# Optimization experiments

Hardware: AMD Instinct MI355X
Metric: run time of the kernel (lower is better)

## Reference

```python
import jax, jax.numpy as jnp
import numpy as np

B, S, DIM, H = 4, 2048, 1024, 16
HD = DIM // H
SCALE = HD ** -0.5


def setup_inputs() -> dict:
    key = jax.random.key(0)
    ks = jax.random.split(key, 7)
    init = 0.02
    return {
        "query": jax.random.normal(ks[0], (B, S, DIM), dtype=jnp.float32),
        "key": jax.random.normal(ks[1], (B, S, DIM), dtype=jnp.float32),
        "value": jax.random.normal(ks[2], (B, S, DIM), dtype=jnp.float32),
        "attn_mask": jnp.tril(jnp.ones((S, S), dtype=bool)),
        "Wq": jax.random.normal(ks[3], (DIM, DIM), dtype=jnp.float32) * init,
        "Wk": jax.random.normal(ks[4], (DIM, DIM), dtype=jnp.float32) * init,
        "Wv": jax.random.normal(ks[5], (DIM, DIM), dtype=jnp.float32) * init,
        "Wo": jax.random.normal(ks[6], (DIM, DIM), dtype=jnp.float32) * init,
    }


def _heads(x):
    # [B,S,DIM] -> [B,H,S,HD]
    b, s, _ = x.shape
    return x.reshape(b, s, H, HD).transpose(0, 2, 1, 3)


def reference(query, key, value, attn_mask, Wq, Wk, Wv, Wo):
    # nn.Linear: x @ W.T (weights here stored as [out,in])
    q = _heads(query @ Wq.T)
    k = _heads(key @ Wk.T)
    v = _heads(value @ Wv.T)
    logits = jnp.einsum("bhqd,bhkd->bhqk", q, k) * SCALE
    mask = attn_mask[None, None, :, :]  # broadcast to [B,H,S,S]
    masked = jnp.where(mask, logits, -1e9)
    weights = jax.nn.softmax(masked, axis=-1)
    weights = weights * mask.astype(weights.dtype)
    denom = jnp.maximum(weights.sum(axis=-1, keepdims=True), 1e-9)
    weights = weights / denom
    out = jnp.einsum("bhqk,bhkd->bhqd", weights, v)
    out = out.transpose(0, 2, 1, 3).reshape(query.shape[0], query.shape[1], -1)
    return out @ Wo.T
```

## Files before the change

kernel.cpp:

```cpp
#include <hip/hip_runtime.h>
#include <hip/hip_bf16.h>
#include <cstdio>

typedef __attribute__((ext_vector_type(8))) short bf16x8;
typedef __attribute__((ext_vector_type(4))) float f32x4;
typedef unsigned short u16;
typedef unsigned int u32;

__device__ inline u16 f2bf(float f) {
    union { float f; u32 u; } x; x.f = f;
    u32 u = x.u;
    u32 r = (u + 0x7fffu + ((u >> 16) & 1u)) >> 16;
    return (u16)r;
}

__device__ inline float exp2_fast(float x) {
    float r;
    asm("v_exp_f32 %0, %1" : "=v"(r) : "v"(x));
    return r;
}

__global__ __launch_bounds__(256) void convf2b(const float* __restrict__ s,
                                               u16* __restrict__ d, int n4) {
    int i = blockIdx.x * 256 + threadIdx.x;
    if (i >= n4) return;
    float4 v = reinterpret_cast<const float4*>(s)[i];
    ushort4 o;
    o.x = f2bf(v.x); o.y = f2bf(v.y); o.z = f2bf(v.z); o.w = f2bf(v.w);
    reinterpret_cast<ushort4*>(d)[i] = o;
}

template <int MODE>
__global__ __launch_bounds__(256) void gemm_bt(const u16* __restrict__ A,
                                               const u16* __restrict__ Bw,
                                               void* __restrict__ Cout, float scale) {
    __shared__ u16 As[128 * 64];
    __shared__ u16 Bs[128 * 64];
    const int tid = threadIdx.x;
    const int lane = tid & 63;
    const int w = tid >> 6;
    const int wr = w >> 1, wc = w & 1;
    const int gm = blockIdx.y * 128;
    const int gn = blockIdx.x * 128;

    f32x4 acc[4][4];
#pragma unroll
    for (int m = 0; m < 4; ++m)
#pragma unroll
        for (int n = 0; n < 4; ++n) acc[m][n] = (f32x4){0.f, 0.f, 0.f, 0.f};

    const int srcb = (((lane & 7) ^ ((lane >> 3) & 7)) << 3);
    const int lr8 = lane >> 3;

    for (int k0 = 0; k0 < 1024; k0 += 64) {
#pragma unroll
        for (int jj = 0; jj < 4; ++jj) {
            int j = w * 4 + jj;
            int i = j * 8 + lr8;
            __builtin_amdgcn_global_load_lds(
                (const __attribute__((address_space(1))) void*)(A + (size_t)(gm + i) * 1024 + k0 + srcb),
                (__attribute__((address_space(3))) void*)(As + j * 512), 16, 0, 0);
        }
#pragma unroll
        for (int jj = 0; jj < 4; ++jj) {
            int j = w * 4 + jj;
            int i = j * 8 + lr8;
            __builtin_amdgcn_global_load_lds(
                (const __attribute__((address_space(1))) void*)(Bw + (size_t)(gn + i) * 1024 + k0 + srcb),
                (__attribute__((address_space(3))) void*)(Bs + j * 512), 16, 0, 0);
        }
        __syncthreads();
#pragma unroll
        for (int kk = 0; kk < 2; ++kk) {
            bf16x8 af[4], bfr[4];
            int cb = kk * 4 + (lane >> 4);
#pragma unroll
            for (int m = 0; m < 4; ++m) {
                int r = wr * 64 + m * 16 + (lane & 15);
                af[m] = *reinterpret_cast<const bf16x8*>(&As[r * 64 + ((cb ^ (r & 7)) << 3)]);
            }
#pragma unroll
            for (int n = 0; n < 4; ++n) {
                int r = wc * 64 + n * 16 + (lane & 15);
                bfr[n] = *reinterpret_cast<const bf16x8*>(&Bs[r * 64 + ((cb ^ (r & 7)) << 3)]);
            }
#pragma unroll
            for (int m = 0; m < 4; ++m)
#pragma unroll
                for (int n = 0; n < 4; ++n)
                    acc[m][n] = __builtin_amdgcn_mfma_f32_16x16x32_bf16(af[m], bfr[n], acc[m][n], 0, 0, 0);
        }
        __syncthreads();
    }

#pragma unroll
    for (int m = 0; m < 4; ++m) {
#pragma unroll
        for (int n = 0; n < 4; ++n) {
#pragma unroll
            for (int i = 0; i < 4; ++i) {
                int gr = gm + wr * 64 + m * 16 + (lane >> 4) * 4 + i;
                int gc = gn + wc * 64 + n * 16 + (lane & 15);
                float val = acc[m][n][i] * scale;
                if (MODE == 0) {
                    u16* C = (u16*)Cout;
                    int b = gr >> 11, s = gr & 2047, h = gc >> 6, d = gc & 63;
                    C[(size_t)((b * 16 + h) * 2048 + s) * 64 + d] = f2bf(val);
                } else {
                    float* C = (float*)Cout;
                    C[(size_t)gr * 1024 + gc] = val;
                }
            }
        }
    }
}

__global__ __launch_bounds__(256) void attn(const u16* __restrict__ Qp,
                                            const u16* __restrict__ Kp,
                                            const u16* __restrict__ Vp,
                                            u16* __restrict__ O) {
    __shared__ u16 Ks[2][64 * 64];
    __shared__ u16 Vt[2][64 * 64];
    __shared__ u16 Ps[4][16 * 64];
    const int tid = threadIdx.x;
    const int lane = tid & 63;
    const int w = tid >> 6;
    const int flat = blockIdx.x;
    const int qi = 31 - (flat >> 6);
    const int bh = flat & 63;
    const int q0 = qi * 64;
    const int qbase = q0 + w * 16;
    const size_t hb = (size_t)bh * 2048;

    bf16x8 aq[2];
    {
        int r = qbase + (lane & 15);
        const u16* qrow = Qp + (hb + r) * 64;
        aq[0] = *reinterpret_cast<const bf16x8*>(qrow + 8 * (lane >> 4));
        aq[1] = *reinterpret_cast<const bf16x8*>(qrow + 32 + 8 * (lane >> 4));
    }

    f32x4 oacc[4];
#pragma unroll
    for (int nt = 0; nt < 4; ++nt) oacc[nt] = (f32x4){0.f, 0.f, 0.f, 0.f};
    float lrow[4] = {0.f, 0.f, 0.f, 0.f};

    const int srcb = (((lane & 7) ^ ((lane >> 3) & 7)) << 3);
    const int lr8 = lane >> 3;
    const int vr = (tid >> 3) * 2;
    const int vc0 = (tid & 7) * 8;

    const int ntiles = qi + 1;

    {
#pragma unroll
        for (int jj = 0; jj < 2; ++jj) {
            int j = w * 2 + jj;
            int i = j * 8 + lr8;
            __builtin_amdgcn_global_load_lds(
                (const __attribute__((address_space(1))) void*)(Kp + (hb + i) * 64 + srcb),
                (__attribute__((address_space(3))) void*)(&Ks[0][0] + j * 512), 16, 0, 0);
        }
        const u16* vsrc = Vp + (hb + vr) * 64 + vc0;
        bf16x8 v0 = *reinterpret_cast<const bf16x8*>(vsrc);
        bf16x8 v1 = *reinterpret_cast<const bf16x8*>(vsrc + 64);
#pragma unroll
        for (int j = 0; j < 8; ++j) {
            int d = vc0 + j;
            u32 pk = (u32)(u16)v0[j] | ((u32)(u16)v1[j] << 16);
            int addr = d * 64 + ((((vr >> 3) ^ (d & 7) ^ ((d >> 3) & 7))) << 3) + (vr & 7);
            *reinterpret_cast<u32*>(&Vt[0][addr]) = pk;
        }
        __syncthreads();
    }

    int cur = 0;
    for (int t = 0; t < ntiles; ++t) {
        const int nxt = cur ^ 1;
        const bool pf = (t + 1 < ntiles);
        bf16x8 nv0, nv1;
        if (pf) {
            int kv1 = (t + 1) * 64;
#pragma unroll
            for (int jj = 0; jj < 2; ++jj) {
                int j = w * 2 + jj;
                int i = j * 8 + lr8;
                __builtin_amdgcn_global_load_lds(
                    (const __attribute__((address_space(1))) void*)(Kp + (hb + kv1 + i) * 64 + srcb),
                    (__attribute__((address_space(3))) void*)(&Ks[nxt][0] + j * 512), 16, 0, 0);
            }
            const u16* vsrc = Vp + (hb + kv1 + vr) * 64 + vc0;
            nv0 = *reinterpret_cast<const bf16x8*>(vsrc);
            nv1 = *reinterpret_cast<const bf16x8*>(vsrc + 64);
        }

        f32x4 s[4];
#pragma unroll
        for (int nt = 0; nt < 4; ++nt) s[nt] = (f32x4){0.f, 0.f, 0.f, 0.f};
#pragma unroll
        for (int kk = 0; kk < 2; ++kk) {
            int cb = kk * 4 + (lane >> 4);
#pragma unroll
            for (int nt = 0; nt < 4; ++nt) {
                int r = nt * 16 + (lane & 15);
                bf16x8 kf = *reinterpret_cast<const bf16x8*>(&Ks[cur][r * 64 + ((cb ^ (r & 7)) << 3)]);
                s[nt] = __builtin_amdgcn_mfma_f32_16x16x32_bf16(aq[kk], kf, s[nt], 0, 0, 0);
            }
        }
        if (t == ntiles - 1) {
            int colb = t * 64 + (lane & 15);
            int rowb = qbase + (lane >> 4) * 4;
#pragma unroll
            for (int nt = 0; nt < 4; ++nt)
#pragma unroll
                for (int i = 0; i < 4; ++i)
                    if (colb + nt * 16 > rowb + i) s[nt][i] = -1e30f;
        }
#pragma unroll
        for (int i = 0; i < 4; ++i) {
#pragma unroll
            for (int nt = 0; nt < 4; ++nt) {
                float p = exp2_fast(s[nt][i]);
                s[nt][i] = p;
                lrow[i] += p;
            }
        }
#pragma unroll
        for (int nt = 0; nt < 4; ++nt) {
            int col = nt * 16 + (lane & 15);
#pragma unroll
            for (int i = 0; i < 4; ++i) {
                int row = (lane >> 4) * 4 + i;
                Ps[w][row * 64 + (((col >> 3) ^ (row & 7)) << 3) + (col & 7)] = f2bf(s[nt][i]);
            }
        }
#pragma unroll
        for (int kk = 0; kk < 2; ++kk) {
            int cb = kk * 4 + (lane >> 4);
            int prow = lane & 15;
            bf16x8 pfr = *reinterpret_cast<const bf16x8*>(&Ps[w][prow * 64 + ((cb ^ (prow & 7)) << 3)]);
#pragma unroll
            for (int nt = 0; nt < 4; ++nt) {
                int d = nt * 16 + (lane & 15);
                bf16x8 vf = *reinterpret_cast<const bf16x8*>(
                    &Vt[cur][d * 64 + ((cb ^ (d & 7) ^ ((d >> 3) & 7)) << 3)]);
                oacc[nt] = __builtin_amdgcn_mfma_f32_16x16x32_bf16(pfr, vf, oacc[nt], 0, 0, 0);
            }
        }
        if (pf) {
#pragma unroll
            for (int j = 0; j < 8; ++j) {
                int d = vc0 + j;
                u32 pk = (u32)(u16)nv0[j] | ((u32)(u16)nv1[j] << 16);
                int addr = d * 64 + ((((vr >> 3) ^ (d & 7) ^ ((d >> 3) & 7))) << 3) + (vr & 7);
                *reinterpret_cast<u32*>(&Vt[nxt][addr]) = pk;
            }
        }
        __syncthreads();
        cur = nxt;
    }

#pragma unroll
    for (int i = 0; i < 4; ++i) {
        lrow[i] += __shfl_xor(lrow[i], 1);
        lrow[i] += __shfl_xor(lrow[i], 2);
        lrow[i] += __shfl_xor(lrow[i], 4);
        lrow[i] += __shfl_xor(lrow[i], 8);
    }
    int b = bh >> 4, h = bh & 15;
#pragma unroll
    for (int i = 0; i < 4; ++i) {
        float inv = 1.0f / lrow[i];
        int srow = qbase + (lane >> 4) * 4 + i;
        size_t base = ((size_t)(b * 2048) + srow) * 1024 + h * 64;
#pragma unroll
        for (int nt = 0; nt < 4; ++nt) {
            int d = nt * 16 + (lane & 15);
            O[base + d] = f2bf(oacc[nt][i] * inv);
        }
    }
}

extern "C" void kernel_launch(void* const* d_in, const int* in_sizes, int n_in,
                              void* d_out, int out_size, void* d_ws, size_t ws_size,
                              hipStream_t stream) {
    const float* q  = (const float*)d_in[0];
    const float* k  = (const float*)d_in[1];
    const float* v  = (const float*)d_in[2];
    const float* Wq = (const float*)d_in[4];
    const float* Wk = (const float*)d_in[5];
    const float* Wv = (const float*)d_in[6];
    const float* Wo = (const float*)d_in[7];
    float* out = (float*)d_out;

    const size_t MB16 = 16777216;
    const size_t WSZ  = 2097152;
    const size_t need = 4 * MB16 + 4 * WSZ;
    if (ws_size < need) {
        fprintf(stderr, "kernel_launch: ws too small (%zu < %zu)\n", ws_size, need);
        return;
    }
    char* ws = (char*)d_ws;
    u16* Xa  = (u16*)(ws + 0 * MB16);
    u16* Qp  = (u16*)(ws + 1 * MB16);
    u16* Kp  = (u16*)(ws + 2 * MB16);
    u16* Vp  = (u16*)(ws + 3 * MB16);
    u16* Wqb = (u16*)(ws + 4 * MB16 + 0 * WSZ);
    u16* Wkb = (u16*)(ws + 4 * MB16 + 1 * WSZ);
    u16* Wvb = (u16*)(ws + 4 * MB16 + 2 * WSZ);
    u16* Wob = (u16*)(ws + 4 * MB16 + 3 * WSZ);

    const int n4x = 8388608 / 4;
    const int n4w = 1048576 / 4;
    dim3 ggrid(8, 64);

    convf2b<<<(n4w + 255) / 256, 256, 0, stream>>>(Wq, Wqb, n4w);
    convf2b<<<(n4w + 255) / 256, 256, 0, stream>>>(Wk, Wkb, n4w);
    convf2b<<<(n4w + 255) / 256, 256, 0, stream>>>(Wv, Wvb, n4w);
    convf2b<<<(n4w + 255) / 256, 256, 0, stream>>>(Wo, Wob, n4w);

    convf2b<<<(n4x + 255) / 256, 256, 0, stream>>>(q, Xa, n4x);
    gemm_bt<0><<<ggrid, 256, 0, stream>>>(Xa, Wqb, Qp, 0.125f * 1.44269504f);

    convf2b<<<(n4x + 255) / 256, 256, 0, stream>>>(k, Xa, n4x);
    gemm_bt<0><<<ggrid, 256, 0, stream>>>(Xa, Wkb, Kp, 1.0f);

    convf2b<<<(n4x + 255) / 256, 256, 0, stream>>>(v, Xa, n4x);
    gemm_bt<0><<<ggrid, 256, 0, stream>>>(Xa, Wvb, Vp, 1.0f);

    attn<<<dim3(2048), 256, 0, stream>>>(Qp, Kp, Vp, Xa);

    gemm_bt<1><<<ggrid, 256, 0, stream>>>(Xa, Wob, out, 1.0f);
}
```

Before: 347.3 us.

## Fuse fp32-to-bf16 conversion into QKV GEMM and keep P in registers

Merges the four weight conversions into one launch. Folds the fp32-to-bf16 activation conversion into a single batched QKV projection kernel that reads fp32 directly and packs it into LDS. In attention, the QK product is transposed so P stays in registers and is redistributed with ds_bpermute instead of a round trip through shared memory. It also swaps the grid axes for the GEMMs. This removes the separate conversion passes and several launches, at the cost of fp32 A loads that are synchronous rather than async-to-LDS inside the GEMM loop.

```diff
diff --git a/kernel.cpp b/kernel.cpp
--- a/kernel.cpp
+++ b/kernel.cpp
@@ -20,14 +20,113 @@
     return r;
 }
 
-__global__ __launch_bounds__(256) void convf2b(const float* __restrict__ s,
-                                               u16* __restrict__ d, int n4) {
+__device__ inline int cvt_pk_bf16(float lo, float hi) {
+    int r;
+    asm("v_cvt_pk_bf16_f32 %0, %1, %2" : "=v"(r) : "v"(lo), "v"(hi));
+    return r;
+}
+
+__global__ __launch_bounds__(256) void convw(const float* __restrict__ w0, const float* __restrict__ w1,
+                                             const float* __restrict__ w2, const float* __restrict__ w3,
+                                             u16* __restrict__ o0, u16* __restrict__ o1,
+                                             u16* __restrict__ o2, u16* __restrict__ o3) {
     int i = blockIdx.x * 256 + threadIdx.x;
-    if (i >= n4) return;
-    float4 v = reinterpret_cast<const float4*>(s)[i];
+    int seg = i >> 18, off = i & 262143;
+    const float* s = seg == 0 ? w0 : seg == 1 ? w1 : seg == 2 ? w2 : w3;
+    u16* d = seg == 0 ? o0 : seg == 1 ? o1 : seg == 2 ? o2 : o3;
+    float4 v = reinterpret_cast<const float4*>(s)[off];
     ushort4 o;
     o.x = f2bf(v.x); o.y = f2bf(v.y); o.z = f2bf(v.z); o.w = f2bf(v.w);
-    reinterpret_cast<ushort4*>(d)[i] = o;
+    reinterpret_cast<ushort4*>(d)[off] = o;
+}
+
+__global__ __launch_bounds__(256) void gemm_qkv(
+        const float* __restrict__ X0, const float* __restrict__ X1, const float* __restrict__ X2,
+        const u16* __restrict__ W0, const u16* __restrict__ W1, const u16* __restrict__ W2,
+        u16* __restrict__ C0, u16* __restrict__ C1, u16* __restrict__ C2, float qscale) {
+    const int z = blockIdx.z;
+    const float* A32 = (z == 0) ? X0 : (z == 1) ? X1 : X2;
+    const u16*  Bw   = (z == 0) ? W0 : (z == 1) ? W1 : W2;
+    u16*        C    = (z == 0) ? C0 : (z == 1) ? C1 : C2;
+    const float scale = (z == 0) ? qscale : 1.0f;
+
+    __shared__ u16 As[128 * 64];
+    __shared__ u16 Bs[128 * 64];
+    const int tid = threadIdx.x;
+    const int lane = tid & 63;
+    const int w = tid >> 6;
+    const int wr = w >> 1, wc = w & 1;
+    const int gm = blockIdx.x * 128;
+    const int gn = blockIdx.y * 128;
+
+    f32x4 acc[4][4];
+#pragma unroll
+    for (int m = 0; m < 4; ++m)
+#pragma unroll
+        for (int n = 0; n < 4; ++n) acc[m][n] = (f32x4){0.f, 0.f, 0.f, 0.f};
+
+    const int srcb = (((lane & 7) ^ ((lane >> 3) & 7)) << 3);
+    const int lr8 = lane >> 3;
+
+    for (int k0 = 0; k0 < 1024; k0 += 64) {
+#pragma unroll
+        for (int jj = 0; jj < 4; ++jj) {
+            int j = w * 4 + jj;
+            int i = j * 8 + lr8;
+            __builtin_amdgcn_global_load_lds(
+                (const __attribute__((address_space(1))) void*)(Bw + (size_t)(gn + i) * 1024 + k0 + srcb),
+                (__attribute__((address_space(3))) void*)(Bs + j * 512), 16, 0, 0);
+        }
+#pragma unroll
+        for (int cc = 0; cc < 4; ++cc) {
+            int cid = cc * 256 + tid;
+            int r = cid >> 3, cb = cid & 7;
+            const float* src = A32 + (size_t)(gm + r) * 1024 + k0 + cb * 8;
+            float4 f0 = *reinterpret_cast<const float4*>(src);
+            float4 f1 = *reinterpret_cast<const float4*>(src + 4);
+            int4 pkd;
+            pkd.x = cvt_pk_bf16(f0.x, f0.y);
+            pkd.y = cvt_pk_bf16(f0.z, f0.w);
+            pkd.z = cvt_pk_bf16(f1.x, f1.y);
+            pkd.w = cvt_pk_bf16(f1.z, f1.w);
+            *reinterpret_cast<int4*>(&As[r * 64 + ((cb ^ (r & 7)) << 3)]) = pkd;
+        }
+        __syncthreads();
+#pragma unroll
+        for (int kk = 0; kk < 2; ++kk) {
+            bf16x8 af[4], bfr[4];
+            int cb = kk * 4 + (lane >> 4);
+#pragma unroll
+            for (int m = 0; m < 4; ++m) {
+                int r = wr * 64 + m * 16 + (lane & 15);
+                af[m] = *reinterpret_cast<const bf16x8*>(&As[r * 64 + ((cb ^ (r & 7)) << 3)]);
+            }
+#pragma unroll
+            for (int n = 0; n < 4; ++n) {
+                int r = wc * 64 + n * 16 + (lane & 15);
+                bfr[n] = *reinterpret_cast<const bf16x8*>(&Bs[r * 64 + ((cb ^ (r & 7)) << 3)]);
+            }
+#pragma unroll
+            for (int m = 0; m < 4; ++m)
+#pragma unroll
+                for (int n = 0; n < 4; ++n)
+                    acc[m][n] = __builtin_amdgcn_mfma_f32_16x16x32_bf16(af[m], bfr[n], acc[m][n], 0, 0, 0);
+        }
+        __syncthreads();
+    }
+
+#pragma unroll
+    for (int m = 0; m < 4; ++m)
+#pragma unroll
+        for (int n = 0; n < 4; ++n)
+#pragma unroll
+            for (int i = 0; i < 4; ++i) {
+                int gr = gm + wr * 64 + m * 16 + (lane >> 4) * 4 + i;
+                int gc = gn + wc * 64 + n * 16 + (lane & 15);
+                float val = acc[m][n][i] * scale;
+                int b = gr >> 11, s = gr & 2047, h = gc >> 6, d = gc & 63;
+                C[(size_t)((b * 16 + h) * 2048 + s) * 64 + d] = f2bf(val);
+            }
 }
 
 template <int MODE>
@@ -40,8 +139,8 @@
     const int lane = tid & 63;
     const int w = tid >> 6;
     const int wr = w >> 1, wc = w & 1;
-    const int gm = blockIdx.y * 128;
-    const int gn = blockIdx.x * 128;
+    const int gm = blockIdx.x * 128;
+    const int gn = blockIdx.y * 128;
 
     f32x4 acc[4][4];
 #pragma unroll
@@ -94,9 +193,9 @@
     }
 
 #pragma unroll
-    for (int m = 0; m < 4; ++m) {
-#pragma unroll
-        for (int n = 0; n < 4; ++n) {
+    for (int m = 0; m < 4; ++m)
+#pragma unroll
+        for (int n = 0; n < 4; ++n)
 #pragma unroll
             for (int i = 0; i < 4; ++i) {
                 int gr = gm + wr * 64 + m * 16 + (lane >> 4) * 4 + i;
@@ -111,8 +210,6 @@
                     C[(size_t)gr * 1024 + gc] = val;
                 }
             }
-        }
-    }
 }
 
 __global__ __launch_bounds__(256) void attn(const u16* __restrict__ Qp,
@@ -121,10 +218,11 @@
                                             u16* __restrict__ O) {
     __shared__ u16 Ks[2][64 * 64];
     __shared__ u16 Vt[2][64 * 64];
-    __shared__ u16 Ps[4][16 * 64];
     const int tid = threadIdx.x;
     const int lane = tid & 63;
     const int w = tid >> 6;
+    const int g = lane >> 4;
+    const int qc = lane & 15;
     const int flat = blockIdx.x;
     const int qi = 31 - (flat >> 6);
     const int bh = flat & 63;
@@ -134,21 +232,26 @@
 
     bf16x8 aq[2];
     {
-        int r = qbase + (lane & 15);
+        int r = qbase + qc;
         const u16* qrow = Qp + (hb + r) * 64;
-        aq[0] = *reinterpret_cast<const bf16x8*>(qrow + 8 * (lane >> 4));
-        aq[1] = *reinterpret_cast<const bf16x8*>(qrow + 32 + 8 * (lane >> 4));
+        aq[0] = *reinterpret_cast<const bf16x8*>(qrow + 8 * g);
+        aq[1] = *reinterpret_cast<const bf16x8*>(qrow + 32 + 8 * g);
     }
 
     f32x4 oacc[4];
 #pragma unroll
     for (int nt = 0; nt < 4; ++nt) oacc[nt] = (f32x4){0.f, 0.f, 0.f, 0.f};
-    float lrow[4] = {0.f, 0.f, 0.f, 0.f};
+    float lsum = 0.f;
 
     const int srcb = (((lane & 7) ^ ((lane >> 3) & 7)) << 3);
     const int lr8 = lane >> 3;
     const int vr = (tid >> 3) * 2;
     const int vc0 = (tid & 7) * 8;
+
+    const int idxA = (qc + ((lane & 16) << 1)) << 2;
+    const int idxB = idxA + 64;
+    const bool hihalf = (lane >= 32);
+    const int qq = w * 16 + qc;
 
     const int ntiles = qi + 1;
 
@@ -199,83 +302,89 @@
         for (int nt = 0; nt < 4; ++nt) s[nt] = (f32x4){0.f, 0.f, 0.f, 0.f};
 #pragma unroll
         for (int kk = 0; kk < 2; ++kk) {
-            int cb = kk * 4 + (lane >> 4);
+            int cb = kk * 4 + g;
 #pragma unroll
             for (int nt = 0; nt < 4; ++nt) {
-                int r = nt * 16 + (lane & 15);
+                int r = nt * 16 + qc;
                 bf16x8 kf = *reinterpret_cast<const bf16x8*>(&Ks[cur][r * 64 + ((cb ^ (r & 7)) << 3)]);
-                s[nt] = __builtin_amdgcn_mfma_f32_16x16x32_bf16(aq[kk], kf, s[nt], 0, 0, 0);
+                s[nt] = __builtin_amdgcn_mfma_f32_16x16x32_bf16(kf, aq[kk], s[nt], 0, 0, 0);
             }
         }
         if (t == ntiles - 1) {
-            int colb = t * 64 + (lane & 15);
-            int rowb = qbase + (lane >> 4) * 4;
 #pragma unroll
             for (int nt = 0; nt < 4; ++nt)
 #pragma unroll
                 for (int i = 0; i < 4; ++i)
-                    if (colb + nt * 16 > rowb + i) s[nt][i] = -1e30f;
-        }
-#pragma unroll
-        for (int i = 0; i < 4; ++i) {
-#pragma unroll
-            for (int nt = 0; nt < 4; ++nt) {
+                    if (nt * 16 + 4 * g + i > qq) s[nt][i] = -1e30f;
+        }
+#pragma unroll
+        for (int nt = 0; nt < 4; ++nt)
+#pragma unroll
+            for (int i = 0; i < 4; ++i) {
                 float p = exp2_fast(s[nt][i]);
                 s[nt][i] = p;
-                lrow[i] += p;
-            }
-        }
+                lsum += p;
+            }
+        int pk[4][2];
 #pragma unroll
         for (int nt = 0; nt < 4; ++nt) {
-            int col = nt * 16 + (lane & 15);
-#pragma unroll
-            for (int i = 0; i < 4; ++i) {
-                int row = (lane >> 4) * 4 + i;
-                Ps[w][row * 64 + (((col >> 3) ^ (row & 7)) << 3) + (col & 7)] = f2bf(s[nt][i]);
-            }
-        }
+            pk[nt][0] = cvt_pk_bf16(s[nt][0], s[nt][1]);
+            pk[nt][1] = cvt_pk_bf16(s[nt][2], s[nt][3]);
+        }
+        bf16x8 pa[2];
 #pragma unroll
         for (int kk = 0; kk < 2; ++kk) {
-            int cb = kk * 4 + (lane >> 4);
-            int prow = lane & 15;
-            bf16x8 pfr = *reinterpret_cast<const bf16x8*>(&Ps[w][prow * 64 + ((cb ^ (prow & 7)) << 3)]);
+            int a0 = __builtin_amdgcn_ds_bpermute(idxA, pk[2 * kk][0]);
+            int b0 = __builtin_amdgcn_ds_bpermute(idxA, pk[2 * kk + 1][0]);
+            int a1 = __builtin_amdgcn_ds_bpermute(idxA, pk[2 * kk][1]);
+            int b1 = __builtin_amdgcn_ds_bpermute(idxA, pk[2 * kk + 1][1]);
+            int a2 = __builtin_amdgcn_ds_bpermute(idxB, pk[2 * kk][0]);
+            int b2 = __builtin_amdgcn_ds_bpermute(idxB, pk[2 * kk + 1][0]);
+            int a3 = __builtin_amdgcn_ds_bpermute(idxB, pk[2 * kk][1]);
+            int b3 = __builtin_amdgcn_ds_bpermute(idxB, pk[2 * kk + 1][1]);
+            union { int wd[4]; bf16x8 v; } u;
+            u.wd[0] = hihalf ? b0 : a0;
+            u.wd[1] = hihalf ? b1 : a1;
+            u.wd[2] = hihalf ? b2 : a2;
+            u.wd[3] = hihalf ? b3 : a3;
+            pa[kk] = u.v;
+        }
+#pragma unroll
+        for (int kk = 0; kk < 2; ++kk) {
+            int cb = kk * 4 + g;
 #pragma unroll
             for (int nt = 0; nt < 4; ++nt) {
-                int d = nt * 16 + (lane & 15);
+                int d = nt * 16 + qc;
                 bf16x8 vf = *reinterpret_cast<const bf16x8*>(
                     &Vt[cur][d * 64 + ((cb ^ (d & 7) ^ ((d >> 3) & 7)) << 3)]);
-                oacc[nt] = __builtin_amdgcn_mfma_f32_16x16x32_bf16(pfr, vf, oacc[nt], 0, 0, 0);
+                oacc[nt] = __builtin_amdgcn_mfma_f32_16x16x32_bf16(pa[kk], vf, oacc[nt], 0, 0, 0);
             }
         }
         if (pf) {
 #pragma unroll
             for (int j = 0; j < 8; ++j) {
                 int d = vc0 + j;
-                u32 pk = (u32)(u16)nv0[j] | ((u32)(u16)nv1[j] << 16);
+                u32 pkv = (u32)(u16)nv0[j] | ((u32)(u16)nv1[j] << 16);
                 int addr = d * 64 + ((((vr >> 3) ^ (d & 7) ^ ((d >> 3) & 7))) << 3) + (vr & 7);
-                *reinterpret_cast<u32*>(&Vt[nxt][addr]) = pk;
+                *reinterpret_cast<u32*>(&Vt[nxt][addr]) = pkv;
             }
         }
         __syncthreads();
         cur = nxt;
     }
 
+    lsum += __shfl_xor(lsum, 16);
+    lsum += __shfl_xor(lsum, 32);
+    int b = bh >> 4, h = bh & 15;
 #pragma unroll
     for (int i = 0; i < 4; ++i) {
-        lrow[i] += __shfl_xor(lrow[i], 1);
-        lrow[i] += __shfl_xor(lrow[i], 2);
-        lrow[i] += __shfl_xor(lrow[i], 4);
-        lrow[i] += __shfl_xor(lrow[i], 8);
-    }
-    int b = bh >> 4, h = bh & 15;
-#pragma unroll
-    for (int i = 0; i < 4; ++i) {
-        float inv = 1.0f / lrow[i];
-        int srow = qbase + (lane >> 4) * 4 + i;
+        float li = __shfl(lsum, 4 * g + i);
+        float inv = 1.0f / li;
+        int srow = qbase + 4 * g + i;
         size_t base = ((size_t)(b * 2048) + srow) * 1024 + h * 64;
 #pragma unroll
         for (int nt = 0; nt < 4; ++nt) {
-            int d = nt * 16 + (lane & 15);
+            int d = nt * 16 + qc;
             O[base + d] = f2bf(oacc[nt][i] * inv);
         }
     }
@@ -301,34 +410,21 @@
         return;
     }
     char* ws = (char*)d_ws;
-    u16* Xa  = (u16*)(ws + 0 * MB16);
-    u16* Qp  = (u16*)(ws + 1 * MB16);
-    u16* Kp  = (u16*)(ws + 2 * MB16);
-    u16* Vp  = (u16*)(ws + 3 * MB16);
+    u16* Qp  = (u16*)(ws + 0 * MB16);
+    u16* Kp  = (u16*)(ws + 1 * MB16);
+    u16* Vp  = (u16*)(ws + 2 * MB16);
+    u16* O   = (u16*)(ws + 3 * MB16);
     u16* Wqb = (u16*)(ws + 4 * MB16 + 0 * WSZ);
     u16* Wkb = (u16*)(ws + 4 * MB16 + 1 * WSZ);
     u16* Wvb = (u16*)(ws + 4 * MB16 + 2 * WSZ);
     u16* Wob = (u16*)(ws + 4 * MB16 + 3 * WSZ);
 
-    const int n4x = 8388608 / 4;
-    const int n4w = 1048576 / 4;
-    dim3 ggrid(8, 64);
-
-    convf2b<<<(n4w + 255) / 256, 256, 0, stream>>>(Wq, Wqb, n4w);
-    convf2b<<<(n4w + 255) / 256, 256, 0, stream>>>(Wk, Wkb, n4w);
-    convf2b<<<(n4w + 255) / 256, 256, 0, stream>>>(Wv, Wvb, n4w);
-    convf2b<<<(n4w + 255) / 256, 256, 0, stream>>>(Wo, Wob, n4w);
-
-    convf2b<<<(n4x + 255) / 256, 256, 0, stream>>>(q, Xa, n4x);
-    gemm_bt<0><<<ggrid, 256, 0, stream>>>(Xa, Wqb, Qp, 0.125f * 1.44269504f);
-
-    convf2b<<<(n4x + 255) / 256, 256, 0, stream>>>(k, Xa, n4x);
-    gemm_bt<0><<<ggrid, 256, 0, stream>>>(Xa, Wkb, Kp, 1.0f);
-
-    convf2b<<<(n4x + 255) / 256, 256, 0, stream>>>(v, Xa, n4x);
-    gemm_bt<0><<<ggrid, 256, 0, stream>>>(Xa, Wvb, Vp, 1.0f);
-
-    attn<<<dim3(2048), 256, 0, stream>>>(Qp, Kp, Vp, Xa);
-
-    gemm_bt<1><<<ggrid, 256, 0, stream>>>(Xa, Wob, out, 1.0f);
-}
+    convw<<<4096, 256, 0, stream>>>(Wq, Wk, Wv, Wo, Wqb, Wkb, Wvb, Wob);
+
+    gemm_qkv<<<dim3(64, 8, 3), 256, 0, stream>>>(q, k, v, Wqb, Wkb, Wvb, Qp, Kp, Vp,
+                                                 0.125f * 1.44269504f);
+
+    attn<<<dim3(2048), 256, 0, stream>>>(Qp, Kp, Vp, O);
+
+    gemm_bt<1><<<dim3(64, 8), 256, 0, stream>>>(O, Wob, out, 1.0f);
+}
```

Measured after the change: 327.6 us. 5.7% less time.
